# Optimization experiments

Measured on AMD Instinct MI355X. Metric: run time of the kernel, lower is better.

## Reference

```python
import jax, jax.numpy as jnp
import numpy as np

B, T, D, H, L, NS = 256, 256, 128, 512, 3, 24  # batch, seq, input_dim, n_units, num_layers, n_steps


def setup_inputs() -> dict:
    key = jax.random.key(0)
    ks = jax.random.split(key, 1 + 4 * L + 2)
    inp = {"x": jax.random.normal(ks[0], (B, T, D), dtype=jnp.float32)}
    s = 1.0 / np.sqrt(H)  # PyTorch GRU init scale
    i = 1
    for l in range(L):
        din = D if l == 0 else H
        inp[f"w_ih{l}"] = jax.random.uniform(ks[i], (3 * H, din), jnp.float32, -s, s); i += 1
        inp[f"w_hh{l}"] = jax.random.uniform(ks[i], (3 * H, H), jnp.float32, -s, s); i += 1
        inp[f"b_ih{l}"] = jax.random.uniform(ks[i], (3 * H,), jnp.float32, -s, s); i += 1
        inp[f"b_hh{l}"] = jax.random.uniform(ks[i], (3 * H,), jnp.float32, -s, s); i += 1
    sf = 1.0 / np.sqrt(H)
    inp["fc_w"] = jax.random.uniform(ks[i], (NS, H), jnp.float32, -sf, sf)
    inp["fc_b"] = jax.random.uniform(ks[i + 1], (NS,), jnp.float32, -sf, sf)
    return inp


def gru_layer(x, w_ih, w_hh, b_ih, b_hh):
    # x: [B, T, Din] -> [B, T, H]. Gate order (PyTorch): r, z, n.
    gx = jnp.einsum('btd,gd->btg', x, w_ih) + b_ih  # precompute input gates: [B, T, 3H]
    Hd = w_hh.shape[1]

    def step(h, gx_t):
        gh = h @ w_hh.T + b_hh  # [B, 3H]
        xr, xz, xn = jnp.split(gx_t, 3, axis=-1)
        hr, hz, hn = jnp.split(gh, 3, axis=-1)
        r = jax.nn.sigmoid(xr + hr)
        z = jax.nn.sigmoid(xz + hz)
        n = jnp.tanh(xn + r * hn)
        h_new = (1.0 - z) * n + z * h
        return h_new, h_new

    h0 = jnp.zeros((x.shape[0], Hd), dtype=x.dtype)
    _, ys = jax.lax.scan(step, h0, jnp.swapaxes(gx, 0, 1))  # scan over time
    return jnp.swapaxes(ys, 0, 1)  # [B, T, H]


def reference(x, w_ih0, w_hh0, b_ih0, b_hh0, w_ih1, w_hh1, b_ih1, b_hh1,
              w_ih2, w_hh2, b_ih2, b_hh2, fc_w, fc_b):
    h = gru_layer(x, w_ih0, w_hh0, b_ih0, b_hh0)
    h = gru_layer(h, w_ih1, w_hh1, b_ih1, b_hh1)
    h = gru_layer(h, w_ih2, w_hh2, b_ih2, b_hh2)
    return h[:, -1, :] @ fc_w.T + fc_b  # [B, NS]
```

## Files before the change

### kernel.cpp

```cpp
#include <hip/hip_runtime.h>
#include <cstdint>
#include <cstddef>

typedef _Float16 f16;
typedef _Float16 f16x8 __attribute__((ext_vector_type(8)));
typedef float f32x4 __attribute__((ext_vector_type(4)));
typedef unsigned int u32;
typedef unsigned short u16;
typedef u32 u32x4 __attribute__((ext_vector_type(4)));

#define NB 256
#define NT 256
#define ND 128
#define NH 512
#define NG 1536
#define NOUT 24
#define PL (NB * NH)

__device__ __forceinline__ float fsig(float x) {
  float e = __expf(-x);
  return __fdividef(1.0f, 1.0f + e);
}
__device__ __forceinline__ float ftanh(float x) {
  float ax = __builtin_fabsf(x);
  float e = __expf(-2.0f * ax);
  float t = __fdividef(1.0f - e, 1.0f + e);
  return __builtin_copysignf(t, x);
}

__global__ void k_f32_to_f16(const float* __restrict__ in, f16* __restrict__ out, int n) {
  int stride = gridDim.x * blockDim.x;
  for (int i = blockIdx.x * blockDim.x + threadIdx.x; i < n; i += stride)
    out[i] = (f16)in[i];
}

__device__ __forceinline__ void gl16(const f16* g, f16* l) {
  __builtin_amdgcn_global_load_lds(
      (const __attribute__((address_space(1))) u32*)(const void*)g,
      (__attribute__((address_space(3))) u32*)(void*)l, 16, 0, 0);
}

template <int K>
__global__ __launch_bounds__(256) void k_gemm2(
    const f16* __restrict__ A, const f16* __restrict__ W,
    const float* __restrict__ bias, f16* __restrict__ gx, int t0, int tsh) {
  __shared__ f16 As[128 * 32];
  __shared__ f16 Bs[128 * 32];
  const int tid = threadIdx.x;
  const int wave = tid >> 6, lane = tid & 63;
  const int wm = wave >> 1, wn = wave & 1;
  const int m0 = blockIdx.x * 128;
  const int n0 = blockIdx.y * 128;
  const int tmask = (1 << tsh) - 1;

  const int r0 = tid >> 2;
  const int swzs = (r0 >> 1) & 3;
  const int csrc = ((tid & 3) ^ swzs) * 8;
  const int ga0 = m0 + r0, ga1 = m0 + r0 + 64;
  const int gr0 = ((ga0 >> tsh) << 8) + t0 + (ga0 & tmask);
  const int gr1 = ((ga1 >> tsh) << 8) + t0 + (ga1 & tmask);
  const f16* a0 = A + (size_t)gr0 * K + csrc;
  const f16* a1 = A + (size_t)gr1 * K + csrc;
  const f16* b0 = W + (size_t)(n0 + r0) * K + csrc;
  const f16* b1 = W + (size_t)(n0 + r0 + 64) * K + csrc;
  f16* asb = As + wave * 512;
  f16* bsb = Bs + wave * 512;

  const int lr = lane & 15;
  const int kg = lane >> 4;
  const int swzr = ((lr >> 1) & 3);
  const int koff = (kg ^ swzr) * 8;

  f32x4 acc[4][4];
#pragma unroll
  for (int i = 0; i < 4; i++)
#pragma unroll
    for (int j = 0; j < 4; j++) acc[i][j] = (f32x4){0.f, 0.f, 0.f, 0.f};

  for (int k0 = 0; k0 < K; k0 += 32) {
    gl16(a0 + k0, asb);
    gl16(a1 + k0, asb + 2048);
    gl16(b0 + k0, bsb);
    gl16(b1 + k0, bsb + 2048);
    asm volatile("s_waitcnt vmcnt(0)" ::: "memory");
    __syncthreads();
    f16x8 af[4], bf[4];
#pragma unroll
    for (int i = 0; i < 4; i++)
      af[i] = *(const f16x8*)(As + (wm * 64 + i * 16 + lr) * 32 + koff);
#pragma unroll
    for (int j = 0; j < 4; j++)
      bf[j] = *(const f16x8*)(Bs + (wn * 64 + j * 16 + lr) * 32 + koff);
#pragma unroll
    for (int i = 0; i < 4; i++)
#pragma unroll
      for (int j = 0; j < 4; j++)
        acc[i][j] = __builtin_amdgcn_mfma_f32_16x16x32_f16(af[i], bf[j], acc[i][j], 0, 0, 0);
    __syncthreads();
  }
  const int rowb = (lane >> 4) * 4;
#pragma unroll
  for (int j = 0; j < 4; j++) {
    int col = n0 + wn * 64 + j * 16 + lr;
    float bv = bias[col];
#pragma unroll
    for (int i = 0; i < 4; i++) {
      int row = m0 + wm * 64 + i * 16 + rowb;
#pragma unroll
      for (int rr = 0; rr < 4; rr++)
        gx[(size_t)(row + rr) * NG + col] = (f16)(acc[i][j][rr] + bv);
    }
  }
}

#define ISSUE4K(qarr, kkb)                                               \
  _Pragma("unroll") for (int u_ = 0; u_ < 4; u_++) {                     \
    const u32* pp_ = hq + (kkb + u_) * 32 + lkh * 8;                     \
    asm volatile("global_load_dwordx4 %0, %1, off sc0 sc1"               \
                 : "=v"(qarr[2 * u_]) : "v"(pp_));                       \
    asm volatile("global_load_dwordx4 %0, %1, off sc0 sc1"               \
                 : "=v"(qarr[2 * u_ + 1]) : "v"(pp_ + 4));               \
  }

#define CONS4K(qarr, kkb)                                                            \
  _Pragma("unroll") for (int u_ = 0; u_ < 4; u_++) {                                 \
    const int kk_ = kkb + u_;                                                        \
    union { u32 w[4]; f16x8 v; } AH_, AL_;                                           \
    AH_.w[0] = __builtin_amdgcn_perm(qarr[2*u_][1],   qarr[2*u_][0],   0x05040100u); \
    AH_.w[1] = __builtin_amdgcn_perm(qarr[2*u_][3],   qarr[2*u_][2],   0x05040100u); \
    AH_.w[2] = __builtin_amdgcn_perm(qarr[2*u_+1][1], qarr[2*u_+1][0], 0x05040100u); \
    AH_.w[3] = __builtin_amdgcn_perm(qarr[2*u_+1][3], qarr[2*u_+1][2], 0x05040100u); \
    AL_.w[0] = __builtin_amdgcn_perm(qarr[2*u_][1],   qarr[2*u_][0],   0x07060302u); \
    AL_.w[1] = __builtin_amdgcn_perm(qarr[2*u_][3],   qarr[2*u_][2],   0x07060302u); \
    AL_.w[2] = __builtin_amdgcn_perm(qarr[2*u_+1][1], qarr[2*u_+1][0], 0x07060302u); \
    AL_.w[3] = __builtin_amdgcn_perm(qarr[2*u_+1][3], qarr[2*u_+1][2], 0x07060302u); \
    const int co_ = (((kk_ * 4 + lkh) ^ swz) << 3);                                  \
    f16x8 bro_ = *(const f16x8*)(wro_ + co_);                                        \
    f16x8 bzo_ = *(const f16x8*)(wzo_ + co_);                                        \
    f16x8 bno_ = *(const f16x8*)(wno_ + co_);                                        \
    f16x8 brx_ = *(const f16x8*)(wrx_ + co_);                                        \
    f16x8 bzx_ = *(const f16x8*)(wzx_ + co_);                                        \
    f16x8 bnx_ = *(const f16x8*)(wnx_ + co_);                                        \
    aRo = __builtin_amdgcn_mfma_f32_16x16x32_f16(AH_.v, bro_, aRo, 0, 0, 0);         \
    aZo = __builtin_amdgcn_mfma_f32_16x16x32_f16(AH_.v, bzo_, aZo, 0, 0, 0);         \
    aNo = __builtin_amdgcn_mfma_f32_16x16x32_f16(AH_.v, bno_, aNo, 0, 0, 0);         \
    aRx = __builtin_amdgcn_mfma_f32_16x16x32_f16(AH_.v, brx_, aRx, 0, 0, 0);         \
    aZx = __builtin_amdgcn_mfma_f32_16x16x32_f16(AH_.v, bzx_, aZx, 0, 0, 0);         \
    aNx = __builtin_amdgcn_mfma_f32_16x16x32_f16(AH_.v, bnx_, aNx, 0, 0, 0);         \
    aRo = __builtin_amdgcn_mfma_f32_16x16x32_f16(AL_.v, bro_, aRo, 0, 0, 0);         \
    aZo = __builtin_amdgcn_mfma_f32_16x16x32_f16(AL_.v, bzo_, aZo, 0, 0, 0);         \
    aNo = __builtin_amdgcn_mfma_f32_16x16x32_f16(AL_.v, bno_, aNo, 0, 0, 0);         \
    aRx = __builtin_amdgcn_mfma_f32_16x16x32_f16(AL_.v, brx_, aRx, 0, 0, 0);         \
    aZx = __builtin_amdgcn_mfma_f32_16x16x32_f16(AL_.v, bzx_, aZx, 0, 0, 0);         \
    aNx = __builtin_amdgcn_mfma_f32_16x16x32_f16(AL_.v, bnx_, aNx, 0, 0, 0);         \
  }

struct RecUnit {
  const f16* gx; const f16* whh; const float* bhh;
  u32* exq; u32* fl; int t0; int bar_base;
};

__global__ __launch_bounds__(256, 1) void k_rec(
    RecUnit u0, RecUnit u1, f16* __restrict__ h, int Tc) {
  __shared__ f16 wlds[96 * 512];
  __shared__ float plds[2][2][64][12];
  const RecUnit U = (blockIdx.x < 128) ? u0 : u1;
  const int bid = blockIdx.x & 127;
  const f16* __restrict__ gx = U.gx;
  u32* __restrict__ exq = U.exq;
  const int t0 = U.t0, bar_base = U.bar_base;
  const int tid = threadIdx.x;
  const int g = bid >> 4;
  const int cs = bid & 15;
  const int b0 = g * 32, c0 = cs * 32;
  const int lane = tid & 63, wave = tid >> 6;
  const int wm = wave >> 1, ks = wave & 1;
  const int lr = lane & 15, lkh = lane >> 4;
  const int first = (t0 == 0) ? 1 : 0;

  for (int idx = tid; idx < 96 * 64; idx += 256) {
    int lrw = idx >> 6, c = idx & 63;
    int grow = (lrw >> 5) * NH + c0 + (lrw & 31);
    f16x8 v = *(const f16x8*)(U.whh + (size_t)grow * NH + c * 8);
    *(f16x8*)(wlds + lrw * 512 + ((c ^ (lrw & 7)) << 3)) = v;
  }
  __syncthreads();

  const int jo = ks * 16 + lr;
  const int jx = (1 - ks) * 16 + lr;
  const int j = c0 + jo;
  const float bh_r = U.bhh[j], bh_z = U.bhh[NH + j], bh_n = U.bhh[2 * NH + j];
  const int arow = b0 + wm * 16 + lr;
  const int rowbase = b0 + wm * 16 + lkh * 4;
  const int swz = lr & 7;
  const f16* wro_ = wlds + jo * 512;
  const f16* wzo_ = wlds + (32 + jo) * 512;
  const f16* wno_ = wlds + (64 + jo) * 512;
  const f16* wrx_ = wlds + jx * 512;
  const f16* wzx_ = wlds + (32 + jx) * 512;
  const f16* wnx_ = wlds + (64 + jx) * 512;
  const int ks8 = ks * 8;
  u32* myflag = U.fl + g * 64 + cs;
  u32* gflags = U.fl + g * 64;
  const int pl = lane & 15;

  union PK2 { u32 u; f16 hh[2]; };

  float hold[4];
  if (first) {
#pragma unroll
    for (int r = 0; r < 4; r++) hold[r] = 0.f;
  } else {
#pragma unroll
    for (int r = 0; r < 4; r++) {
      PK2 pk;
      pk.u = __hip_atomic_load(exq + (size_t)(rowbase + r) * NH + j,
                               __ATOMIC_RELAXED, __HIP_MEMORY_SCOPE_AGENT);
      hold[r] = (float)pk.hh[0] + (float)pk.hh[1];
    }
  }

  float xr[4], xz[4], xn[4];
#pragma unroll
  for (int r = 0; r < 4; r++) {
    const f16* gp = gx + ((size_t)(rowbase + r) * Tc) * NG + j;
    xr[r] = (float)gp[0]; xz[r] = (float)gp[NH]; xn[r] = (float)gp[2 * NH];
  }

  int cur = 0;
  for (int t = 0; t < Tc; t++) {
    f32x4 aRo = {0.f, 0.f, 0.f, 0.f}, aZo = {0.f, 0.f, 0.f, 0.f}, aNo = {0.f, 0.f, 0.f, 0.f};
    f32x4 aRx = {0.f, 0.f, 0.f, 0.f}, aZx = {0.f, 0.f, 0.f, 0.f}, aNx = {0.f, 0.f, 0.f, 0.f};
    if (t > 0 || !first) {
      const u32* hq = exq + (size_t)cur * PL + (size_t)arow * NH;
      u32x4 q0[8], q1[8];
      ISSUE4K(q0, ks8);
      ISSUE4K(q1, ks8 + 4);
      asm volatile("s_waitcnt vmcnt(8)" ::: "memory");
      __builtin_amdgcn_sched_barrier(0);
      CONS4K(q0, ks8);
      asm volatile("s_waitcnt vmcnt(0)" ::: "memory");
      __builtin_amdgcn_sched_barrier(0);
      CONS4K(q1, ks8 + 4);
      float* ps = &plds[wm][ks][lane][0];
#pragma unroll
      for (int i = 0; i < 4; i++) {
        ps[i] = aRx[i]; ps[4 + i] = aZx[i]; ps[8 + i] = aNx[i];
      }
      __syncthreads();
      const float* pr = &plds[wm][1 - ks][lane][0];
#pragma unroll
      for (int i = 0; i < 4; i++) {
        aRo[i] += pr[i]; aZo[i] += pr[4 + i]; aNo[i] += pr[8 + i];
      }
    }
    u32* outq = exq + (size_t)(cur ^ 1) * PL;
    f16 hhi_s[4];
#pragma unroll
    for (int r = 0; r < 4; r++) {
      float rg = fsig(xr[r] + aRo[r] + bh_r);
      float zg = fsig(xz[r] + aZo[r] + bh_z);
      float ng = ftanh(xn[r] + rg * (aNo[r] + bh_n));
      float hnew = ng + zg * (hold[r] - ng);
      hold[r] = hnew;
      PK2 pk;
      pk.hh[0] = (f16)hnew;
      pk.hh[1] = (f16)(hnew - (float)pk.hh[0]);
      hhi_s[r] = pk.hh[0];
      __hip_atomic_store(outq + (size_t)(rowbase + r) * NH + j, pk.u,
                         __ATOMIC_RELAXED, __HIP_MEMORY_SCOPE_AGENT);
    }
    if (t < Tc - 1) {
      asm volatile("s_waitcnt vmcnt(0)" ::: "memory");
      __syncthreads();
      if (tid == 0)
        __hip_atomic_store(myflag, (u32)(bar_base + t + 1),
                           __ATOMIC_RELAXED, __HIP_MEMORY_SCOPE_AGENT);
#pragma unroll
      for (int r = 0; r < 4; r++)
        h[((size_t)(rowbase + r) * NT + (t0 + t)) * NH + j] = hhi_s[r];
#pragma unroll
      for (int r = 0; r < 4; r++) {
        const f16* gp = gx + ((size_t)(rowbase + r) * Tc + (t + 1)) * NG + j;
        xr[r] = (float)gp[0]; xz[r] = (float)gp[NH]; xn[r] = (float)gp[2 * NH];
      }
      asm volatile("" ::: "memory");
      const u32 target = (u32)(bar_base + t + 1);
      for (;;) {
        u32 v = __hip_atomic_load(gflags + pl,
                                  __ATOMIC_RELAXED, __HIP_MEMORY_SCOPE_AGENT);
        if (__all(v >= target)) break;
        __builtin_amdgcn_s_sleep(1);
      }
      asm volatile("" ::: "memory");
    } else {
#pragma unroll
      for (int r = 0; r < 4; r++)
        h[((size_t)(rowbase + r) * NT + (t0 + t)) * NH + j] = hhi_s[r];
    }
    cur ^= 1;
  }
}

__global__ void k_fc(const f16* __restrict__ h, const float* __restrict__ fcw,
                     const float* __restrict__ fcb, float* __restrict__ out) {
  int b = blockIdx.x;
  int lane = threadIdx.x;
  __shared__ float hrow[NH];
  for (int k = lane; k < NH; k += 64)
    hrow[k] = (float)h[((size_t)b * NT + (NT - 1)) * NH + k];
  __syncthreads();
  for (int o = 0; o < NOUT; o++) {
    float sm = 0.f;
    for (int k = lane; k < NH; k += 64) sm += hrow[k] * fcw[o * NH + k];
#pragma unroll
    for (int off = 32; off; off >>= 1) sm += __shfl_down(sm, off);
    if (lane == 0) out[b * NOUT + o] = sm + fcb[o];
  }
}

extern "C" void kernel_launch(void* const* d_in, const int* in_sizes, int n_in,
                              void* d_out, int out_size, void* d_ws, size_t ws_size,
                              hipStream_t stream) {
  (void)in_sizes; (void)n_in; (void)out_size;
  const float* x = (const float*)d_in[0];
  const float* w_ih[3] = {(const float*)d_in[1], (const float*)d_in[5], (const float*)d_in[9]};
  const float* w_hh[3] = {(const float*)d_in[2], (const float*)d_in[6], (const float*)d_in[10]};
  const float* b_ih[3] = {(const float*)d_in[3], (const float*)d_in[7], (const float*)d_in[11]};
  const float* b_hh[3] = {(const float*)d_in[4], (const float*)d_in[8], (const float*)d_in[12]};
  const float* fcw = (const float*)d_in[13];
  const float* fcb = (const float*)d_in[14];

  const size_t fixed = 32768 +
                       ((size_t)NG * ND + 2 * (size_t)NG * NH) * 2  +
                       3 * (size_t)NG * NH * 2  +
                       (size_t)NB * NT * ND * 2  +
                       (size_t)NB * NT * NH * 2  +
                       3 * (size_t)2 * PL * 4 ;
  int Tc = 64;
  while (Tc > 16 && fixed + 2 * ((size_t)NB * Tc * NG * 2) > ws_size) Tc >>= 1;
  const int nc = NT / Tc;
  int tsh = 0;
  while ((1 << tsh) < Tc) tsh++;

  char* p = (char*)d_ws;
  size_t off = 0;
  u32* ctrl = (u32*)(p + off); off += 32768;
  f16* wih_f[3]; f16* whh_f[3];
  const int wih_sz[3] = {NG * ND, NG * NH, NG * NH};
  for (int l = 0; l < 3; l++) {
    wih_f[l] = (f16*)(p + off); off += (size_t)wih_sz[l] * 2;
    whh_f[l] = (f16*)(p + off); off += (size_t)NG * NH * 2;
  }
  f16* xf16 = (f16*)(p + off); off += (size_t)NB * NT * ND * 2;
  f16* h = (f16*)(p + off); off += (size_t)NB * NT * NH * 2;
  u32* exq[3];
  for (int l = 0; l < 3; l++) {
    exq[l] = (u32*)(p + off); off += (size_t)2 * PL * 4;
  }
  f16* gxbuf[2];
  for (int s = 0; s < 2; s++) {
    gxbuf[s] = (f16*)(p + off); off += (size_t)NB * Tc * NG * 2;
  }

  hipMemsetAsync(ctrl, 0, 32768, stream);

  auto conv = [&](const float* src, f16* dst, int n) {
    int blocks = (n + 1023) / 1024; if (blocks > 2048) blocks = 2048;
    k_f32_to_f16<<<dim3(blocks), dim3(256), 0, stream>>>(src, dst, n);
  };
  conv(x, xf16, NB * NT * ND);
  for (int l = 0; l < 3; l++) {
    conv(w_ih[l], wih_f[l], wih_sz[l]);
    conv(w_hh[l], whh_f[l], NG * NH);
  }

  const int mblocks = (NB * Tc) / 128;

  bool done[3][16] = {};
  int completed = 0, total = 3 * nc;
  while (completed < total) {
    int pl_[2], pc_[2], np = 0;
    bool picked[3][16] = {};
    for (int s = 0; s < 2; s++) {
      int bl = -1, bc = -1, bk = 1 << 30;
      for (int l = 0; l < 3; l++)
        for (int c = 0; c < nc; c++) {
          if (done[l][c] || picked[l][c]) continue;
          if (l > 0 && !done[l - 1][c]) continue;
          if (c > 0 && !done[l][c - 1]) continue;
          int key = (l + c) * 4 + l;
          if (key < bk) { bk = key; bl = l; bc = c; }
        }
      if (bl < 0) break;
      picked[bl][bc] = true;
      pl_[np] = bl; pc_[np] = bc; np++;
    }
    for (int s = 0; s < np; s++) {
      int l = pl_[s], c = pc_[s];
      if (l == 0)
        k_gemm2<ND><<<dim3(mblocks, 12), dim3(256), 0, stream>>>(
            xf16, wih_f[0], b_ih[0], gxbuf[s], c * Tc, tsh);
      else
        k_gemm2<NH><<<dim3(mblocks, 12), dim3(256), 0, stream>>>(
            h, wih_f[l], b_ih[l], gxbuf[s], c * Tc, tsh);
    }
    RecUnit us[2];
    for (int s = 0; s < np; s++) {
      int l = pl_[s], c = pc_[s];
      us[s].gx = gxbuf[s];
      us[s].whh = whh_f[l];
      us[s].bhh = b_hh[l];
      us[s].exq = exq[l];
      us[s].fl = ctrl + l * 512;
      us[s].t0 = c * Tc;
      us[s].bar_base = c * (Tc - 1);
    }
    if (np == 1) us[1] = us[0];
    k_rec<<<dim3(np * 128), dim3(256), 0, stream>>>(us[0], us[1], h, Tc);
    for (int s = 0; s < np; s++) { done[pl_[s]][pc_[s]] = true; completed++; }
  }
  k_fc<<<dim3(NB), dim3(64), 0, stream>>>(h, fcw, fcb, (float*)d_out);
}
```

Before: 2.668 ms.

## Run all three GRU layers concurrently in a diagonal wavefront schedule

The recurrent kernel now takes three work units, so each launch runs the chunk of all three layers that lie on one anti-diagonal (layer l, chunk d-l). Before, at most two layers ran at once under a greedy picker. To fit 384 blocks with two blocks per CU, the n-gate slice of W_hh is kept in registers instead of LDS. That shrinks LDS from 96 to 64 rows and raises launch bounds to 2 blocks per CU. The trade-offs are more register pressure, a third gx buffer that may force a smaller time chunk, and co-resident blocks contending for the CU.

```diff
diff --git a/kernel.cpp b/kernel.cpp
--- a/kernel.cpp
+++ b/kernel.cpp
@@ -122,7 +122,7 @@
                  : "=v"(qarr[2 * u_ + 1]) : "v"(pp_ + 4));               \
   }
 
-#define CONS4K(qarr, kkb)                                                            \
+#define CONS4K(qarr, kkb, nb0)                                                       \
   _Pragma("unroll") for (int u_ = 0; u_ < 4; u_++) {                                 \
     const int kk_ = kkb + u_;                                                        \
     union { u32 w[4]; f16x8 v; } AH_, AL_;                                           \
@@ -137,10 +137,10 @@
     const int co_ = (((kk_ * 4 + lkh) ^ swz) << 3);                                  \
     f16x8 bro_ = *(const f16x8*)(wro_ + co_);                                        \
     f16x8 bzo_ = *(const f16x8*)(wzo_ + co_);                                        \
-    f16x8 bno_ = *(const f16x8*)(wno_ + co_);                                        \
     f16x8 brx_ = *(const f16x8*)(wrx_ + co_);                                        \
     f16x8 bzx_ = *(const f16x8*)(wzx_ + co_);                                        \
-    f16x8 bnx_ = *(const f16x8*)(wnx_ + co_);                                        \
+    f16x8 bno_ = bnO[nb0 + u_];                                                      \
+    f16x8 bnx_ = bnX[nb0 + u_];                                                      \
     aRo = __builtin_amdgcn_mfma_f32_16x16x32_f16(AH_.v, bro_, aRo, 0, 0, 0);         \
     aZo = __builtin_amdgcn_mfma_f32_16x16x32_f16(AH_.v, bzo_, aZo, 0, 0, 0);         \
     aNo = __builtin_amdgcn_mfma_f32_16x16x32_f16(AH_.v, bno_, aNo, 0, 0, 0);         \
@@ -160,11 +160,14 @@
   u32* exq; u32* fl; int t0; int bar_base;
 };
 
-__global__ __launch_bounds__(256, 1) void k_rec(
-    RecUnit u0, RecUnit u1, f16* __restrict__ h, int Tc) {
-  __shared__ f16 wlds[96 * 512];
+__global__ __launch_bounds__(256, 2) void k_rec(
+    RecUnit u0, RecUnit u1, RecUnit u2, f16* __restrict__ h, int Tc) {
+  __shared__ f16 wlds[64 * 512];
   __shared__ float plds[2][2][64][12];
-  const RecUnit U = (blockIdx.x < 128) ? u0 : u1;
+  RecUnit U = u0;
+  const int ui = blockIdx.x >> 7;
+  if (ui == 1) U = u1;
+  if (ui == 2) U = u2;
   const int bid = blockIdx.x & 127;
   const f16* __restrict__ gx = U.gx;
   u32* __restrict__ exq = U.exq;
@@ -177,8 +180,22 @@
   const int wm = wave >> 1, ks = wave & 1;
   const int lr = lane & 15, lkh = lane >> 4;
   const int first = (t0 == 0) ? 1 : 0;
-
-  for (int idx = tid; idx < 96 * 64; idx += 256) {
+  const int jo = ks * 16 + lr;
+  const int jx = (1 - ks) * 16 + lr;
+  const int ks8 = ks * 8;
+
+  f16x8 bnO[8], bnX[8];
+  {
+    const f16* wb = U.whh + (size_t)(2 * NH + c0) * NH + (size_t)ks8 * 32 + lkh * 8;
+    const f16* wO = wb + (size_t)jo * NH;
+    const f16* wX = wb + (size_t)jx * NH;
+#pragma unroll
+    for (int i = 0; i < 8; i++) {
+      bnO[i] = *(const f16x8*)(wO + i * 32);
+      bnX[i] = *(const f16x8*)(wX + i * 32);
+    }
+  }
+  for (int idx = tid; idx < 64 * 64; idx += 256) {
     int lrw = idx >> 6, c = idx & 63;
     int grow = (lrw >> 5) * NH + c0 + (lrw & 31);
     f16x8 v = *(const f16x8*)(U.whh + (size_t)grow * NH + c * 8);
@@ -186,8 +203,6 @@
   }
   __syncthreads();
 
-  const int jo = ks * 16 + lr;
-  const int jx = (1 - ks) * 16 + lr;
   const int j = c0 + jo;
   const float bh_r = U.bhh[j], bh_z = U.bhh[NH + j], bh_n = U.bhh[2 * NH + j];
   const int arow = b0 + wm * 16 + lr;
@@ -195,11 +210,8 @@
   const int swz = lr & 7;
   const f16* wro_ = wlds + jo * 512;
   const f16* wzo_ = wlds + (32 + jo) * 512;
-  const f16* wno_ = wlds + (64 + jo) * 512;
   const f16* wrx_ = wlds + jx * 512;
   const f16* wzx_ = wlds + (32 + jx) * 512;
-  const f16* wnx_ = wlds + (64 + jx) * 512;
-  const int ks8 = ks * 8;
   u32* myflag = U.fl + g * 64 + cs;
   u32* gflags = U.fl + g * 64;
   const int pl = lane & 15;
@@ -238,10 +250,10 @@
       ISSUE4K(q1, ks8 + 4);
       asm volatile("s_waitcnt vmcnt(8)" ::: "memory");
       __builtin_amdgcn_sched_barrier(0);
-      CONS4K(q0, ks8);
+      CONS4K(q0, ks8, 0);
       asm volatile("s_waitcnt vmcnt(0)" ::: "memory");
       __builtin_amdgcn_sched_barrier(0);
-      CONS4K(q1, ks8 + 4);
+      CONS4K(q1, ks8 + 4, 4);
       float* ps = &plds[wm][ks][lane][0];
 #pragma unroll
       for (int i = 0; i < 4; i++) {
@@ -338,7 +350,7 @@
                        (size_t)NB * NT * NH * 2  +
                        3 * (size_t)2 * PL * 4 ;
   int Tc = 64;
-  while (Tc > 16 && fixed + 2 * ((size_t)NB * Tc * NG * 2) > ws_size) Tc >>= 1;
+  while (Tc > 16 && fixed + 3 * ((size_t)NB * Tc * NG * 2) > ws_size) Tc >>= 1;
   const int nc = NT / Tc;
   int tsh = 0;
   while ((1 << tsh) < Tc) tsh++;
@@ -358,8 +370,8 @@
   for (int l = 0; l < 3; l++) {
     exq[l] = (u32*)(p + off); off += (size_t)2 * PL * 4;
   }
-  f16* gxbuf[2];
-  for (int s = 0; s < 2; s++) {
+  f16* gxbuf[3];
+  for (int s = 0; s < 3; s++) {
     gxbuf[s] = (f16*)(p + off); off += (size_t)NB * Tc * NG * 2;
   }
 
@@ -377,25 +389,14 @@
 
   const int mblocks = (NB * Tc) / 128;
 
-  bool done[3][16] = {};
-  int completed = 0, total = 3 * nc;
-  while (completed < total) {
-    int pl_[2], pc_[2], np = 0;
-    bool picked[3][16] = {};
-    for (int s = 0; s < 2; s++) {
-      int bl = -1, bc = -1, bk = 1 << 30;
-      for (int l = 0; l < 3; l++)
-        for (int c = 0; c < nc; c++) {
-          if (done[l][c] || picked[l][c]) continue;
-          if (l > 0 && !done[l - 1][c]) continue;
-          if (c > 0 && !done[l][c - 1]) continue;
-          int key = (l + c) * 4 + l;
-          if (key < bk) { bk = key; bl = l; bc = c; }
-        }
-      if (bl < 0) break;
-      picked[bl][bc] = true;
-      pl_[np] = bl; pc_[np] = bc; np++;
-    }
+  for (int d = 0; d < 3 + nc - 1; d++) {
+    int pl_[3], pc_[3], np = 0;
+    for (int l = 0; l < 3; l++) {
+      int c = d - l;
+      if (c < 0 || c >= nc) continue;
+      pl_[np] = l; pc_[np] = c; np++;
+    }
+    if (np == 0) continue;
     for (int s = 0; s < np; s++) {
       int l = pl_[s], c = pc_[s];
       if (l == 0)
@@ -405,7 +406,7 @@
         k_gemm2<NH><<<dim3(mblocks, 12), dim3(256), 0, stream>>>(
             h, wih_f[l], b_ih[l], gxbuf[s], c * Tc, tsh);
     }
-    RecUnit us[2];
+    RecUnit us[3];
     for (int s = 0; s < np; s++) {
       int l = pl_[s], c = pc_[s];
       us[s].gx = gxbuf[s];
@@ -416,9 +417,8 @@
       us[s].t0 = c * Tc;
       us[s].bar_base = c * (Tc - 1);
     }
-    if (np == 1) us[1] = us[0];
-    k_rec<<<dim3(np * 128), dim3(256), 0, stream>>>(us[0], us[1], h, Tc);
-    for (int s = 0; s < np; s++) { done[pl_[s]][pc_[s]] = true; completed++; }
+    for (int s = np; s < 3; s++) us[s] = us[0];
+    k_rec<<<dim3(np * 128), dim3(256), 0, stream>>>(us[0], us[1], us[2], h, Tc);
   }
   k_fc<<<dim3(NB), dim3(64), 0, stream>>>(h, fcw, fcb, (float*)d_out);
 }
```

New measurement: 2.556 ms. 4.2% less time.
